# Optimization experiments

Measured on AMD Instinct MI355X. Metric: run time of the kernel, lower is better.

The kernel has to match this reference:

```python
import jax, jax.numpy as jnp
import numpy as np
from jax import lax

START_ID = 0
END_ID = 1
NUM_TAGS = 128
B, T = 512, 512
NEG = -10000.0


def setup_inputs() -> dict:
    key = jax.random.key(0)
    k1, k2, k3 = jax.random.split(key, 3)
    x = jax.random.normal(k1, (B, T, NUM_TAGS), dtype=jnp.float32)
    tags = jax.random.randint(k2, (B, T + 1), 0, NUM_TAGS)
    tags = tags.at[:, 0].set(START_ID)  # gold path starts at start tag
    mask = jnp.ones((B, T), dtype=jnp.float32)
    # xavier-normal std = sqrt(2/(fan_in+fan_out))
    std = np.sqrt(2.0 / (NUM_TAGS + NUM_TAGS))
    transition = jax.random.normal(k3, (NUM_TAGS, NUM_TAGS), dtype=jnp.float32) * std
    return {"x": x, "tags": tags, "mask": mask, "transition": transition}


def _forward_alg(x, mask, transition):
    # x: [B, T, K] emissions; transition[j, k]: score k -> j
    b, t, k = x.shape
    alpha0 = jnp.full((b, k), NEG, dtype=x.dtype).at[:, START_ID].set(0.0)

    def step(alpha, inp):
        emit, m = inp  # emit [B, K], m [B]
        # scores[b, j, k] = alpha[b, k] + emit[b, j] + transition[j, k]
        scores = alpha[:, None, :] + emit[:, :, None] + transition[None, :, :]
        new_alpha = jax.nn.logsumexp(scores, axis=2)  # [B, K]
        alpha = jnp.where(m[:, None] > 0, new_alpha, alpha)
        return alpha, None

    alpha, _ = lax.scan(step, alpha0, (x.transpose(1, 0, 2), mask.T))
    return jax.nn.logsumexp(alpha + transition[END_ID][None, :], axis=1)  # [B]


def _gold_score(x, tags, mask, transition):
    # emission at gold next tags: [B, T]
    emit = jnp.take_along_axis(x, tags[:, 1:, None], axis=2)[..., 0]
    # transition tags[t] -> tags[t+1]: [B, T]
    trans = transition[tags[:, 1:], tags[:, :-1]]
    score = jnp.sum((emit + trans) * mask, axis=1)
    lengths = jnp.sum(mask, axis=1).astype(jnp.int32)  # [B]
    last_tag = jnp.take_along_axis(tags, lengths[:, None], axis=1)[:, 0]
    return score + transition[END_ID, last_tag]


def reference(x, tags, mask, transition):
    forward_score = _forward_alg(x, mask, transition)
    gold_score = _gold_score(x, tags, mask, transition)
    return forward_score - gold_score  # [B] per-sequence NLL
```

## Files before the change

### kernel.cpp

```cpp
#include <hip/hip_runtime.h>
#include <hip/hip_bf16.h>

#define NTAGS 128
#define TLEN 512
#define BATCH 512
#define START_ID 0
#define END_ID 1

#define REP16(M) M(0) M(1) M(2) M(3) M(4) M(5) M(6) M(7) \
                 M(8) M(9) M(10) M(11) M(12) M(13) M(14) M(15)

__global__ __launch_bounds__(256, 2) void k_crf(
    const float* __restrict__ x, const int* __restrict__ tags,
    const float* __restrict__ mask, const float* __restrict__ transition,
    float* __restrict__ out)
{
  const int b = blockIdx.x;
  const int j = threadIdx.x;
  const int r = j >> 1;
  const int h = j & 1;

  __shared__ __align__(16) float p_lds[2][NTAGS];
  __shared__ float red_lds[8];

  const float* xb = x + (size_t)b * TLEN * NTAGS;
  const float* mb = mask + b * TLEN;
  const int*   tb = tags + b * (TLEN + 1);

  float gs = 0.f, msum = 0.f;
  #pragma unroll
  for (int rr = 0; rr < 2; ++rr) {
    int t = j + rr * 256;
    int to = tb[t + 1];
    int from = tb[t];
    float m = mb[t];
    gs += (xb[(size_t)t * NTAGS + to] + transition[to * NTAGS + from]) * m;
    msum += m;
  }
  #pragma unroll
  for (int off = 32; off > 0; off >>= 1) {
    gs += __shfl_xor(gs, off);
    msum += __shfl_xor(msum, off);
  }
  int wid = j >> 6;
  if ((j & 63) == 0) { red_lds[wid] = gs; red_lds[4 + wid] = msum; }
  __syncthreads();
  float gold_s = 0.f;
  if (j == 0) {
    float gt = red_lds[0] + red_lds[1] + red_lds[2] + red_lds[3];
    int len = (int)(red_lds[4] + red_lds[5] + red_lds[6] + red_lds[7]);
    gold_s = gt + transition[END_ID * NTAGS + tb[len]];
  }

  const float4* trow =
      reinterpret_cast<const float4*>(transition + r * NTAGS + h * 64);
#define E_DECL(n) float4 e##n;
  REP16(E_DECL)
#define E_INIT(n) { float4 tv = trow[n]; \
    e##n.x = __expf(tv.x); e##n.y = __expf(tv.y); \
    e##n.z = __expf(tv.z); e##n.w = __expf(tv.w); }
  REP16(E_INIT)
  const float etend = __expf(transition[END_ID * NTAGS + r]);

  float p = (r == START_ID) ? 1.0f : 0.0f;
  float Clog = 0.0f;
  float s_cur = __expf(xb[r]);
  float m_cur = mb[0];

  int buf = 0;
  for (int t = 0; t < TLEN; ++t) {
    if (h == 0) p_lds[buf][r] = p;
    __syncthreads();

    int tn = (t + 1 < TLEN) ? (t + 1) : (TLEN - 1);
    float emit_nxt = xb[(size_t)tn * NTAGS + r];
    float m_nxt = mb[tn];

    const float4* p4 =
        reinterpret_cast<const float4*>(p_lds[buf]) + h * 16;
    float a0 = 0.f, a1 = 0.f, a2 = 0.f, a3 = 0.f, S = 0.f;
#define E_FMA(n) { float4 pv = p4[n]; \
    a0 = fmaf(pv.x, e##n.x, a0); a1 = fmaf(pv.y, e##n.y, a1); \
    a2 = fmaf(pv.z, e##n.z, a2); a3 = fmaf(pv.w, e##n.w, a3); \
    S += pv.x; }
    REP16(E_FMA)
    float dot = (a0 + a1) + (a2 + a3);
    dot += __shfl_xor(dot, 1);
    S   += __shfl_xor(S, 1);

    float pn = dot * s_cur * (1.0f / S);
    bool upd = (m_cur > 0.0f);
    p = upd ? pn : p;
    Clog += upd ? __logf(S) : 0.0f;

    s_cur = __expf(emit_nxt);
    m_cur = m_nxt;
    buf ^= 1;
  }

  float v = (h == 0) ? p * etend : 0.0f;
  #pragma unroll
  for (int off = 32; off > 0; off >>= 1) v += __shfl_xor(v, off);
  if ((j & 63) == 0) red_lds[wid] = v;
  __syncthreads();
  if (j == 0) {
    float tot = red_lds[0] + red_lds[1] + red_lds[2] + red_lds[3];
    out[b] = Clog + __logf(tot) - gold_s;
  }
}

extern "C" void kernel_launch(void* const* d_in, const int* in_sizes, int n_in,
                              void* d_out, int out_size, void* d_ws, size_t ws_size,
                              hipStream_t stream) {
  const float* x          = (const float*)d_in[0];
  const int*   tags       = (const int*)d_in[1];
  const float* mask       = (const float*)d_in[2];
  const float* transition = (const float*)d_in[3];
  float* out = (float*)d_out;

  k_crf<<<BATCH, 256, 0, stream>>>(x, tags, mask, transition, out);
}
```

Measured before the change: 499.4 us.

## Split each tag row across four lanes with 512-thread blocks and padded LDS

Each output tag is now computed by four threads instead of two, so every thread holds 32 exp-transition values and does half the FMAs per step. Blocks grow to 512 threads. The shared probability vector is stored with padding (36 floats per 32-entry segment) to spread the four lanes' reads across LDS banks. This shortens the serial per-timestep dot-product chain, at the cost of an extra shuffle stage and a larger barrier across 8 waves every step.

```diff
diff --git a/kernel.cpp b/kernel.cpp
--- a/kernel.cpp
+++ b/kernel.cpp
@@ -7,59 +7,59 @@
 #define START_ID 0
 #define END_ID 1
 
-#define REP16(M) M(0) M(1) M(2) M(3) M(4) M(5) M(6) M(7) \
-                 M(8) M(9) M(10) M(11) M(12) M(13) M(14) M(15)
+#define REP8(M) M(0) M(1) M(2) M(3) M(4) M(5) M(6) M(7)
 
-__global__ __launch_bounds__(256, 2) void k_crf(
+__global__ __launch_bounds__(512)
+__attribute__((amdgpu_waves_per_eu(4, 4)))
+void k_crf(
     const float* __restrict__ x, const int* __restrict__ tags,
     const float* __restrict__ mask, const float* __restrict__ transition,
     float* __restrict__ out)
 {
   const int b = blockIdx.x;
   const int j = threadIdx.x;
-  const int r = j >> 1;
-  const int h = j & 1;
+  const int r = j >> 2;
+  const int q = j & 3;
 
-  __shared__ __align__(16) float p_lds[2][NTAGS];
-  __shared__ float red_lds[8];
+  __shared__ __align__(16) float p_lds[2][144];
+  __shared__ float red_lds[16];
 
   const float* xb = x + (size_t)b * TLEN * NTAGS;
   const float* mb = mask + b * TLEN;
   const int*   tb = tags + b * (TLEN + 1);
 
-  float gs = 0.f, msum = 0.f;
-  #pragma unroll
-  for (int rr = 0; rr < 2; ++rr) {
-    int t = j + rr * 256;
-    int to = tb[t + 1];
-    int from = tb[t];
-    float m = mb[t];
-    gs += (xb[(size_t)t * NTAGS + to] + transition[to * NTAGS + from]) * m;
-    msum += m;
+  {
+    int to = tb[j + 1];
+    int from = tb[j];
+    float m = mb[j];
+    float gs = (xb[(size_t)j * NTAGS + to] + transition[to * NTAGS + from]) * m;
+    float msum = m;
+    #pragma unroll
+    for (int off = 32; off > 0; off >>= 1) {
+      gs += __shfl_xor(gs, off);
+      msum += __shfl_xor(msum, off);
+    }
+    int wid = j >> 6;
+    if ((j & 63) == 0) { red_lds[wid] = gs; red_lds[8 + wid] = msum; }
   }
-  #pragma unroll
-  for (int off = 32; off > 0; off >>= 1) {
-    gs += __shfl_xor(gs, off);
-    msum += __shfl_xor(msum, off);
-  }
-  int wid = j >> 6;
-  if ((j & 63) == 0) { red_lds[wid] = gs; red_lds[4 + wid] = msum; }
   __syncthreads();
   float gold_s = 0.f;
   if (j == 0) {
-    float gt = red_lds[0] + red_lds[1] + red_lds[2] + red_lds[3];
-    int len = (int)(red_lds[4] + red_lds[5] + red_lds[6] + red_lds[7]);
+    float gt = 0.f, lt = 0.f;
+    #pragma unroll
+    for (int w = 0; w < 8; ++w) { gt += red_lds[w]; lt += red_lds[8 + w]; }
+    int len = (int)lt;
     gold_s = gt + transition[END_ID * NTAGS + tb[len]];
   }
 
   const float4* trow =
-      reinterpret_cast<const float4*>(transition + r * NTAGS + h * 64);
+      reinterpret_cast<const float4*>(transition + r * NTAGS + q * 32);
 #define E_DECL(n) float4 e##n;
-  REP16(E_DECL)
+  REP8(E_DECL)
 #define E_INIT(n) { float4 tv = trow[n]; \
     e##n.x = __expf(tv.x); e##n.y = __expf(tv.y); \
     e##n.z = __expf(tv.z); e##n.w = __expf(tv.w); }
-  REP16(E_INIT)
+  REP8(E_INIT)
   const float etend = __expf(transition[END_ID * NTAGS + r]);
 
   float p = (r == START_ID) ? 1.0f : 0.0f;
@@ -67,9 +67,10 @@
   float s_cur = __expf(xb[r]);
   float m_cur = mb[0];
 
+  const int widx = (r >> 5) * 36 + (r & 31);
   int buf = 0;
   for (int t = 0; t < TLEN; ++t) {
-    if (h == 0) p_lds[buf][r] = p;
+    if (q == 0) p_lds[buf][widx] = p;
     __syncthreads();
 
     int tn = (t + 1 < TLEN) ? (t + 1) : (TLEN - 1);
@@ -77,16 +78,18 @@
     float m_nxt = mb[tn];
 
     const float4* p4 =
-        reinterpret_cast<const float4*>(p_lds[buf]) + h * 16;
+        reinterpret_cast<const float4*>(p_lds[buf]) + q * 9;
     float a0 = 0.f, a1 = 0.f, a2 = 0.f, a3 = 0.f, S = 0.f;
 #define E_FMA(n) { float4 pv = p4[n]; \
     a0 = fmaf(pv.x, e##n.x, a0); a1 = fmaf(pv.y, e##n.y, a1); \
     a2 = fmaf(pv.z, e##n.z, a2); a3 = fmaf(pv.w, e##n.w, a3); \
     S += pv.x; }
-    REP16(E_FMA)
+    REP8(E_FMA)
     float dot = (a0 + a1) + (a2 + a3);
     dot += __shfl_xor(dot, 1);
-    S   += __shfl_xor(S, 1);
+    dot += __shfl_xor(dot, 2);
+    S += __shfl_xor(S, 1);
+    S += __shfl_xor(S, 2);
 
     float pn = dot * s_cur * (1.0f / S);
     bool upd = (m_cur > 0.0f);
@@ -98,13 +101,15 @@
     buf ^= 1;
   }
 
-  float v = (h == 0) ? p * etend : 0.0f;
+  float v = (q == 0) ? p * etend : 0.0f;
   #pragma unroll
   for (int off = 32; off > 0; off >>= 1) v += __shfl_xor(v, off);
-  if ((j & 63) == 0) red_lds[wid] = v;
+  if ((j & 63) == 0) red_lds[j >> 6] = v;
   __syncthreads();
   if (j == 0) {
-    float tot = red_lds[0] + red_lds[1] + red_lds[2] + red_lds[3];
+    float tot = 0.f;
+    #pragma unroll
+    for (int w = 0; w < 8; ++w) tot += red_lds[w];
     out[b] = Clog + __logf(tot) - gold_s;
   }
 }
@@ -118,5 +123,5 @@
   const float* transition = (const float*)d_in[3];
   float* out = (float*)d_out;
 
-  k_crf<<<BATCH, 256, 0, stream>>>(x, tags, mask, transition, out);
+  k_crf<<<BATCH, 512, 0, stream>>>(x, tags, mask, transition, out);
 }
```

Result: slower. 525.3 us (+5.2%).

## Normalize by START tag probability, pad LDS, prefetch emissions and mask

Applied to the files above, without the earlier changes.

The per-step normalizer changes from a partial sum of probabilities, which needed extra adds and a cross-lane shuffle, to a single LDS read of p[0]. The reciprocal becomes a hardware rcp. The probability buffer in LDS is padded so the two half-rows fall in different banks. The mask is staged once into LDS, and emissions are prefetched two steps ahead, to shorten the serial critical path of each recurrence step. Normalizing by one element is mathematically valid, but it relies on p[0] staying well scaled, which could affect numerical robustness.

```diff
diff --git a/kernel.cpp b/kernel.cpp
--- a/kernel.cpp
+++ b/kernel.cpp
@@ -1,5 +1,4 @@
 #include <hip/hip_runtime.h>
-#include <hip/hip_bf16.h>
 
 #define NTAGS 128
 #define TLEN 512
@@ -10,7 +9,9 @@
 #define REP16(M) M(0) M(1) M(2) M(3) M(4) M(5) M(6) M(7) \
                  M(8) M(9) M(10) M(11) M(12) M(13) M(14) M(15)
 
-__global__ __launch_bounds__(256, 2) void k_crf(
+__global__ __launch_bounds__(256)
+__attribute__((amdgpu_waves_per_eu(2, 2)))
+void k_crf(
     const float* __restrict__ x, const int* __restrict__ tags,
     const float* __restrict__ mask, const float* __restrict__ transition,
     float* __restrict__ out)
@@ -20,30 +21,35 @@
   const int r = j >> 1;
   const int h = j & 1;
 
-  __shared__ __align__(16) float p_lds[2][NTAGS];
+  __shared__ __align__(16) float p_lds[2][136];
+  __shared__ float m_lds[TLEN];
   __shared__ float red_lds[8];
 
   const float* xb = x + (size_t)b * TLEN * NTAGS;
   const float* mb = mask + b * TLEN;
   const int*   tb = tags + b * (TLEN + 1);
 
-  float gs = 0.f, msum = 0.f;
-  #pragma unroll
-  for (int rr = 0; rr < 2; ++rr) {
-    int t = j + rr * 256;
-    int to = tb[t + 1];
-    int from = tb[t];
-    float m = mb[t];
-    gs += (xb[(size_t)t * NTAGS + to] + transition[to * NTAGS + from]) * m;
-    msum += m;
+  {
+    float m0 = mb[j], m1 = mb[j + 256];
+    m_lds[j] = m0; m_lds[j + 256] = m1;
+    float gs = 0.f, msum = 0.f;
+    #pragma unroll
+    for (int rr = 0; rr < 2; ++rr) {
+      int t = j + rr * 256;
+      float m = (rr == 0) ? m0 : m1;
+      int to = tb[t + 1];
+      int from = tb[t];
+      gs += (xb[(size_t)t * NTAGS + to] + transition[to * NTAGS + from]) * m;
+      msum += m;
+    }
+    #pragma unroll
+    for (int off = 32; off > 0; off >>= 1) {
+      gs += __shfl_xor(gs, off);
+      msum += __shfl_xor(msum, off);
+    }
+    int wid = j >> 6;
+    if ((j & 63) == 0) { red_lds[wid] = gs; red_lds[4 + wid] = msum; }
   }
-  #pragma unroll
-  for (int off = 32; off > 0; off >>= 1) {
-    gs += __shfl_xor(gs, off);
-    msum += __shfl_xor(msum, off);
-  }
-  int wid = j >> 6;
-  if ((j & 63) == 0) { red_lds[wid] = gs; red_lds[4 + wid] = msum; }
   __syncthreads();
   float gold_s = 0.f;
   if (j == 0) {
@@ -64,44 +70,46 @@
 
   float p = (r == START_ID) ? 1.0f : 0.0f;
   float Clog = 0.0f;
-  float s_cur = __expf(xb[r]);
-  float m_cur = mb[0];
+  const float* pe = xb + r;
+  float s_cur = __expf(pe[0]);
+  float em1 = pe[NTAGS];
+  pe += 2 * NTAGS;
 
+  const int wslot = (r >> 6) * 68 + (r & 63);
   int buf = 0;
   for (int t = 0; t < TLEN; ++t) {
-    if (h == 0) p_lds[buf][r] = p;
+    if (h == 0) p_lds[buf][wslot] = p;
     __syncthreads();
 
-    int tn = (t + 1 < TLEN) ? (t + 1) : (TLEN - 1);
-    float emit_nxt = xb[(size_t)tn * NTAGS + r];
-    float m_nxt = mb[tn];
+    float em2 = (t + 2 < TLEN) ? pe[0] : 0.f;
+    float m_cur = m_lds[t];
 
     const float4* p4 =
-        reinterpret_cast<const float4*>(p_lds[buf]) + h * 16;
-    float a0 = 0.f, a1 = 0.f, a2 = 0.f, a3 = 0.f, S = 0.f;
+        reinterpret_cast<const float4*>(p_lds[buf]) + h * 17;
+    float a0 = 0.f, a1 = 0.f, a2 = 0.f, a3 = 0.f;
 #define E_FMA(n) { float4 pv = p4[n]; \
     a0 = fmaf(pv.x, e##n.x, a0); a1 = fmaf(pv.y, e##n.y, a1); \
-    a2 = fmaf(pv.z, e##n.z, a2); a3 = fmaf(pv.w, e##n.w, a3); \
-    S += pv.x; }
+    a2 = fmaf(pv.z, e##n.z, a2); a3 = fmaf(pv.w, e##n.w, a3); }
     REP16(E_FMA)
     float dot = (a0 + a1) + (a2 + a3);
     dot += __shfl_xor(dot, 1);
-    S   += __shfl_xor(S, 1);
 
-    float pn = dot * s_cur * (1.0f / S);
+    float S = p_lds[buf][0];
+    float pn = dot * s_cur * __builtin_amdgcn_rcpf(S);
     bool upd = (m_cur > 0.0f);
     p = upd ? pn : p;
     Clog += upd ? __logf(S) : 0.0f;
 
-    s_cur = __expf(emit_nxt);
-    m_cur = m_nxt;
+    s_cur = __expf(em1);
+    em1 = em2;
+    pe += NTAGS;
     buf ^= 1;
   }
 
   float v = (h == 0) ? p * etend : 0.0f;
   #pragma unroll
   for (int off = 32; off > 0; off >>= 1) v += __shfl_xor(v, off);
-  if ((j & 63) == 0) red_lds[wid] = v;
+  if ((j & 63) == 0) red_lds[j >> 6] = v;
   __syncthreads();
   if (j == 0) {
     float tot = red_lds[0] + red_lds[1] + red_lds[2] + red_lds[3];
```

Result: slower. 612.8 us (+22.7%).
